# Kernel optimization log

Hardware: AMD Instinct MI355X
Metric: run time of the kernel (lower is better)

The kernel has to match this reference:

```python
import jax, jax.numpy as jnp
import numpy as np

B, L, H, W = 4, 16, 4096, 128   # W == nfeat == nclass (required by out.reshape)
NHID = 256

def setup_inputs() -> dict:
    key = jax.random.key(0)
    k1, k2, k3, k4 = jax.random.split(key, 4)
    x = jax.random.normal(k1, (B, L, H, W), dtype=jnp.float32)
    # row-normalized-ish dense adjacency stand-in for the sparse normalized adj
    adj = jax.random.uniform(k2, (H, H), dtype=jnp.float32) / H
    # GraphConvolution params: support = input @ Wk; out = adj @ support + bk
    W1 = jax.random.normal(k3, (W, NHID), dtype=jnp.float32) / np.sqrt(W)
    b1 = jnp.zeros((NHID,), dtype=jnp.float32)
    W2 = jax.random.normal(k4, (NHID, W), dtype=jnp.float32) / np.sqrt(NHID)
    b2 = jnp.zeros((W,), dtype=jnp.float32)
    return {"x": x, "adj": adj, "W1": W1, "b1": b1, "W2": W2, "b2": b2}

def reference(x, adj, W1, b1, W2, b2):
    Bv, Lv, Hv, Wv = x.shape
    xf = x.reshape(Bv * Lv, Hv, Wv)                      # [BL, H, F]
    # gc1: transform then aggregate, fused over all slices (replaces per-slice loop)
    h = jnp.einsum('nm,bmf->bnf', adj, xf @ W1) + b1     # [BL, H, nhid]
    h = jax.nn.relu(h)
    # dropout: inference mode (training=False) -> identity
    out = jnp.einsum('nm,bmf->bnf', adj, h @ W2) + b2    # [BL, H, nclass]
    out = out.reshape(Bv, Lv, Hv, Wv)
    return jax.nn.log_softmax(out, axis=-1)
```

## Files before the change

kernel.cpp:

```cpp
#include <hip/hip_runtime.h>

typedef __attribute__((ext_vector_type(4))) float f32x4;
typedef __attribute__((ext_vector_type(16))) float f32x16;
typedef __attribute__((ext_vector_type(4))) int i32x4;
typedef __attribute__((ext_vector_type(8))) int i32x8;
typedef union { i32x8 v8; i32x4 v4[2]; } opnd;

__device__ __forceinline__ unsigned fp4q(float v) {
  float a = __builtin_fabsf(v);
  unsigned q = (unsigned)(a > 0.25f) + (a > 0.75f) + (a > 1.25f) + (a > 1.75f)
             + (a > 2.5f) + (a > 3.5f) + (a > 5.0f);
  return q | (v < 0.0f ? 8u : 0u);
}

#if __has_builtin(__builtin_amdgcn_cvt_scalef32_pk_fp4_f32)
#define PKFP4(old, x, y, s) __builtin_amdgcn_cvt_scalef32_pk_fp4_f32((old), (x), (y), 1.0f, (s))
#else
#define PKFP4(old, x, y, s) ((old) | ((fp4q(x) | (fp4q(y) << 4)) << (8 * (s))))
#endif

__device__ __forceinline__ long tiled_addr(long r, long k, int nkb) {
  return (((r >> 5) * nkb) + (k >> 6)) * 2048 + ((k & 16) ? 1024 : 0)
       + (((r & 31) + (((k >> 5) & 1) << 5)) << 4) + (k & 15);
}
__device__ __forceinline__ long tile4_addr(long r, long k, int nkb) {
  return (((r >> 5) * nkb) + (k >> 6)) * 1024
       + (((r & 31) + (((k >> 5) & 1) << 5)) << 4) + ((k & 31) >> 1);
}

__device__ __forceinline__ long remap_wg(int lin, int nwg, int gx) {
  long g = lin;
  if ((nwg & 7) == 0) {
    int cpx = nwg >> 3;
    int gyx = cpx / gx;
    int xcd = lin & 7, idx = lin >> 3;
    if ((gx & 3) == 0 && gyx >= 4 && (gyx & 3) == 0) {
      int st = idx >> 4, wi = idx & 15;
      int nstr = gx >> 2;
      int str = st % nstr, stc = st / nstr;
      int r = str * 4 + (wi & 3);
      int c2 = stc * 4 + (wi >> 2);
      g = (long)xcd * cpx + (long)c2 * gx + r;
    } else {
      g = (long)xcd * cpx + idx;
    }
  }
  return g;
}

__global__ __launch_bounds__(256) void cvtAdj4t(const float* __restrict__ in,
                                                unsigned char* __restrict__ out, long n) {
  long i = ((long)blockIdx.x * 256 + threadIdx.x) * 8;
  if (i >= n) return;
  float4 a = *(const float4*)(in + i);
  float4 b = *(const float4*)(in + i + 4);
  const float S = 24576.0f;
  unsigned word = PKFP4(0u, a.x * S, a.y * S, 0);
  word = PKFP4(word, a.z * S, a.w * S, 1);
  word = PKFP4(word, b.x * S, b.y * S, 2);
  word = PKFP4(word, b.z * S, b.w * S, 3);
  long r = i >> 12;
  long k = i & 4095;
  *(int*)(out + tile4_addr(r, k, 64)) = (int)word;
}

__global__ __launch_bounds__(256) void cvtX4t(const float* __restrict__ X,
                                              unsigned char* __restrict__ out4) {
  __shared__ float tile[32][33];
  const int tid = threadIdx.x;
  const long bl = blockIdx.z;
  const int m0 = blockIdx.y * 32;
  const int w0 = blockIdx.x * 32;
  const float* xb = X + (bl * 4096 + m0) * 128 + w0;
  int row = tid >> 3, cg = tid & 7;
  float4 v = *(const float4*)(xb + (long)row * 128 + cg * 4);
  tile[row][cg * 4 + 0] = v.x;
  tile[row][cg * 4 + 1] = v.y;
  tile[row][cg * 4 + 2] = v.z;
  tile[row][cg * 4 + 3] = v.w;
  __syncthreads();
  if (tid < 128) {
    int wv = tid & 31, mg = tid >> 5;
    float t[8];
#pragma unroll
    for (int i = 0; i < 8; ++i) t[i] = tile[mg * 8 + i][wv];
    unsigned word = PKFP4(0u, t[0], t[1], 0);
    word = PKFP4(word, t[2], t[3], 1);
    word = PKFP4(word, t[4], t[5], 2);
    word = PKFP4(word, t[6], t[7], 3);
    long r = bl * 128 + w0 + wv;
    long k = m0 + mg * 8;
    *(int*)(out4 + tile4_addr(r, k, 64)) = (int)word;
  }
}

__global__ __launch_bounds__(256) void prep_params(const float* __restrict__ W1,
                                                   const float* __restrict__ W2,
                                                   unsigned char* __restrict__ W1T8,
                                                   unsigned char* __restrict__ W2T8) {
  int idx = blockIdx.x * 256 + threadIdx.x;
  if (idx < 32768) {
    int f = idx >> 7, wv = idx & 127;
    float v = W1[wv * 256 + f] * 16.0f;
    int pk = __builtin_amdgcn_cvt_pk_fp8_f32(v, v, 0, 0);
    W1T8[tiled_addr(f, wv, 2)] = (unsigned char)(pk & 0xff);
  } else {
    int t = idx - 32768;
    int cc = t >> 8, f = t & 255;
    float v = W2[f * 128 + cc] * 16.0f;
    int pk = __builtin_amdgcn_cvt_pk_fp8_f32(v, v, 0, 0);
    W2T8[tiled_addr(cc, f, 4)] = (unsigned char)(pk & 0xff);
  }
}

__global__ __launch_bounds__(256, 3) void gemmS1(const unsigned char* __restrict__ A4,
                                                 const unsigned char* __restrict__ X4,
                                                 const unsigned char* __restrict__ W1T8,
                                                 const unsigned char* __restrict__ W2T8,
                                                 unsigned char* __restrict__ t2T4,
                                                 const float* __restrict__ b1,
                                                 int K, int gx) {
  __shared__ unsigned char lds[49152];
  const int tid = threadIdx.x;
  const int l = tid & 63;
  const int w = tid >> 6;
  long g = remap_wg(blockIdx.x, gridDim.x, gx);
  const long row0 = (g % gx) * 128;
  const long bl = g / gx;
  const int nkb = K >> 6;
  const int wr = w >> 1, wc = w & 1;
  const unsigned char* sAp = A4 + (((row0 >> 5) + w) * (long)nkb) * 1024 + l * 16;
  const unsigned char* sXp = X4 + ((bl * 4 + w) * (long)nkb) * 1024 + l * 16;
  unsigned char* ldsw = lds + w * 1024;
  const unsigned char* rA = lds + (wr * 2) * 1024 + l * 16;
  const unsigned char* rX = lds + 4096 + (wc * 2) * 1024 + l * 16;

  f32x16 acc[2][2] = {};
  opnd aE[2], xE[2], aO[2], xO[2];
  const i32x4 z4 = {0, 0, 0, 0};
#pragma unroll
  for (int fi = 0; fi < 2; ++fi) {
    aE[fi].v4[1] = z4; xE[fi].v4[1] = z4;
    aO[fi].v4[1] = z4; xO[fi].v4[1] = z4;
  }

#define STG(B, SL) do { long o0_ = (long)(2 * (B)) * 1024; long o1_ = o0_ + 1024;     \
    unsigned char* d_ = ldsw + (SL) * 16384;                                          \
    __builtin_amdgcn_global_load_lds((const unsigned int*)(const void*)(sAp + o0_),   \
                                     (unsigned int*)(d_), 16, 0, 0);                  \
    __builtin_amdgcn_global_load_lds((const unsigned int*)(const void*)(sXp + o0_),   \
                                     (unsigned int*)(d_ + 4096), 16, 0, 0);           \
    __builtin_amdgcn_global_load_lds((const unsigned int*)(const void*)(sAp + o1_),   \
                                     (unsigned int*)(d_ + 8192), 16, 0, 0);           \
    __builtin_amdgcn_global_load_lds((const unsigned int*)(const void*)(sXp + o1_),   \
                                     (unsigned int*)(d_ + 12288), 16, 0, 0);          \
  } while (0)
#define LDF(SL, HALF, AV, XV) do { const long s_ = (SL) * 16384 + (HALF) * 8192;      \
    AV[0].v4[0] = *(const i32x4*)(rA + s_);                                           \
    AV[1].v4[0] = *(const i32x4*)(rA + s_ + 1024);                                    \
    XV[0].v4[0] = *(const i32x4*)(rX + s_);                                           \
    XV[1].v4[0] = *(const i32x4*)(rX + s_ + 1024); } while (0)
#define MFMAS(AV, XV) do {                                                            \
    __builtin_amdgcn_s_setprio(1);                                                    \
    _Pragma("unroll") for (int fi = 0; fi < 2; ++fi)                                  \
      _Pragma("unroll") for (int j = 0; j < 2; ++j)                                   \
        acc[fi][j] = __builtin_amdgcn_mfma_scale_f32_32x32x64_f8f6f4(                 \
            XV[j].v8, AV[fi].v8, acc[fi][j], 4, 4, 0, 127, 0, 124);                   \
    __builtin_amdgcn_s_setprio(0); } while (0)
#define BODYS(SL, SS, DOSTG, B, N) do {                                               \
    LDF(SL, 0, aE, xE);                                                               \
    if (DOSTG) STG((B) + 2, SS);                                                      \
    LDF(SL, 1, aO, xO);                                                               \
    MFMAS(aE, xE);                                                                    \
    MFMAS(aO, xO);                                                                    \
    asm volatile("s_waitcnt vmcnt(" N ")" ::: "memory");                              \
    __builtin_amdgcn_s_barrier(); } while (0)

  STG(0, 0); STG(1, 1);
  asm volatile("s_waitcnt vmcnt(4)" ::: "memory");
  __builtin_amdgcn_s_barrier();
  for (int b = 0; b < 30; b += 3) {
    BODYS(0, 2, 1, b + 0, "4");
    BODYS(1, 0, 1, b + 1, "4");
    BODYS(2, 1, 1, b + 2, "4");
  }
  BODYS(0, 0, 0, 30, "0");
  BODYS(1, 0, 0, 31, "0");
#undef STG
#undef LDF
#undef MFMAS
#undef BODYS

  unsigned char* S1buf = lds;
  unsigned char* hbuf = lds + 16384;

  const int hi = l >> 5;
  const int ln = l & 31;
#pragma unroll
  for (int fi = 0; fi < 2; ++fi) {
    int n = (wr * 2 + fi) * 32 + ln;
#pragma unroll
    for (int j = 0; j < 2; ++j) {
      int wb = (wc * 2 + j) * 32 + 4 * hi;
#pragma unroll
      for (int r4 = 0; r4 < 4; ++r4) {
        int w0 = wb + 8 * r4;
        int word = __builtin_amdgcn_cvt_pk_fp8_f32(acc[fi][j][4 * r4 + 0],
                                                   acc[fi][j][4 * r4 + 1], 0, false);
        word = __builtin_amdgcn_cvt_pk_fp8_f32(acc[fi][j][4 * r4 + 2],
                                               acc[fi][j][4 * r4 + 3], word, true);
        *(int*)(S1buf + tiled_addr(n, w0, 2)) = word;
      }
    }
  }
  __syncthreads();

  const float c1 = 128.0f / 49152.0f;
#pragma unroll
  for (int hh = 0; hh < 2; ++hh) {
#pragma unroll
    for (int fi = 0; fi < 2; ++fi)
#pragma unroll
      for (int jb = 0; jb < 2; ++jb) acc[fi][jb] = (f32x16){};
#pragma unroll
    for (int kt1 = 0; kt1 < 2; ++kt1) {
#pragma unroll
      for (int jb = 0; jb < 2; ++jb) {
        opnd aw;
        const unsigned char* pW = W1T8 + (long)((hh * 4 + wc * 2 + jb) * 2 + kt1) * 2048 + l * 16;
        aw.v4[0] = *(const i32x4*)(pW);
        aw.v4[1] = *(const i32x4*)(pW + 1024);
#pragma unroll
        for (int fi = 0; fi < 2; ++fi) {
          opnd bs;
          const unsigned char* pS = S1buf + (long)((wr * 2 + fi) * 2 + kt1) * 2048 + l * 16;
          bs.v4[0] = *(const i32x4*)(pS);
          bs.v4[1] = *(const i32x4*)(pS + 1024);
          acc[fi][jb] = __builtin_amdgcn_mfma_scale_f32_32x32x64_f8f6f4(
              aw.v8, bs.v8, acc[fi][jb], 0, 0, 0, 127, 0, 127);
        }
      }
    }
#pragma unroll
    for (int jb = 0; jb < 2; ++jb) {
      int fb = (hh * 4 + wc * 2 + jb) * 32 + 4 * hi;
#pragma unroll
      for (int r4 = 0; r4 < 4; ++r4) {
        int f0 = fb + 8 * r4;
        float4 bb = *(const float4*)(b1 + f0);
#pragma unroll
        for (int fi = 0; fi < 2; ++fi) {
          int n = (wr * 2 + fi) * 32 + ln;
          float v0 = fmaxf(fmaf(acc[fi][jb][4 * r4 + 0], c1, bb.x * 128.0f), 0.0f);
          float v1 = fmaxf(fmaf(acc[fi][jb][4 * r4 + 1], c1, bb.y * 128.0f), 0.0f);
          float v2 = fmaxf(fmaf(acc[fi][jb][4 * r4 + 2], c1, bb.z * 128.0f), 0.0f);
          float v3 = fmaxf(fmaf(acc[fi][jb][4 * r4 + 3], c1, bb.w * 128.0f), 0.0f);
          int word = __builtin_amdgcn_cvt_pk_fp8_f32(v0, v1, 0, false);
          word = __builtin_amdgcn_cvt_pk_fp8_f32(v2, v3, word, true);
          *(int*)(hbuf + tiled_addr(n, f0, 4)) = word;
        }
      }
    }
  }
  __syncthreads();

#pragma unroll
  for (int fi = 0; fi < 2; ++fi)
#pragma unroll
    for (int jb = 0; jb < 2; ++jb) acc[fi][jb] = (f32x16){};
#pragma unroll
  for (int kt2 = 0; kt2 < 4; ++kt2) {
#pragma unroll
    for (int jb = 0; jb < 2; ++jb) {
      opnd bw;
      const unsigned char* pW = W2T8 + (long)((wc * 2 + jb) * 4 + kt2) * 2048 + l * 16;
      bw.v4[0] = *(const i32x4*)(pW);
      bw.v4[1] = *(const i32x4*)(pW + 1024);
#pragma unroll
      for (int fi = 0; fi < 2; ++fi) {
        opnd ah;
        const unsigned char* pH = hbuf + (long)((wr * 2 + fi) * 4 + kt2) * 2048 + l * 16;
        ah.v4[0] = *(const i32x4*)(pH);
        ah.v4[1] = *(const i32x4*)(pH + 1024);
        acc[fi][jb] = __builtin_amdgcn_mfma_scale_f32_32x32x64_f8f6f4(
            ah.v8, bw.v8, acc[fi][jb], 0, 0, 0, 127, 0, 127);
      }
    }
  }
  unsigned char* ob = t2T4 + bl * 262144;
#pragma unroll
  for (int fi = 0; fi < 2; ++fi) {
#pragma unroll
    for (int jb = 0; jb < 2; ++jb) {
      int cc = wc * 64 + jb * 32 + ln;
#pragma unroll
      for (int run = 0; run < 4; ++run) {
        long n0 = row0 + wr * 64 + fi * 32 + 8 * run + 4 * hi;
        const float s = 0.125f;
        unsigned pkw = PKFP4(0u, acc[fi][jb][run * 4 + 0] * s,
                                 acc[fi][jb][run * 4 + 1] * s, 0);
        pkw = PKFP4(pkw, acc[fi][jb][run * 4 + 2] * s,
                         acc[fi][jb][run * 4 + 3] * s, 1);
        *(ushort*)(ob + tile4_addr(cc, n0, 64)) = (ushort)pkw;
      }
    }
  }
}

__global__ __launch_bounds__(256, 3) void gemm256sm(const unsigned char* __restrict__ A4,
                                                    const unsigned char* __restrict__ B4,
                                                    float* __restrict__ out,
                                                    const float* __restrict__ bias,
                                                    float ooScale, int K, int gx,
                                                    int chunkBase) {
  __shared__ unsigned char lds[49152];
  const int tid = threadIdx.x;
  const int l = tid & 63;
  const int w = tid >> 6;
  long g = remap_wg(blockIdx.x, gridDim.x, gx);
  const long row0 = (g % gx) * 128;
  const long bl = g / gx;
  const int nkb = K >> 6;
  const unsigned char* sAp = A4 + (((row0 >> 5) + w) * (long)nkb) * 1024 + l * 16;
  const unsigned char* sXp = B4 + ((bl * 4 + w) * (long)nkb) * 1024 + l * 16;
  unsigned char* ldsw = lds + w * 1024;
  const unsigned char* rA = lds + w * 1024 + l * 16;
  const unsigned char* rB = lds + 4096 + l * 16;

  f32x16 acc[4] = {};
  opnd aE, aO, bE[4], bO[4];
  const i32x4 z4 = {0, 0, 0, 0};
  aE.v4[1] = z4; aO.v4[1] = z4;
#pragma unroll
  for (int j = 0; j < 4; ++j) { bE[j].v4[1] = z4; bO[j].v4[1] = z4; }

#define STG(B, SL) do { long o0_ = (long)(2 * (B)) * 1024; long o1_ = o0_ + 1024;     \
    unsigned char* d_ = ldsw + (SL) * 16384;                                          \
    __builtin_amdgcn_global_load_lds((const unsigned int*)(const void*)(sAp + o0_),   \
                                     (unsigned int*)(d_), 16, 0, 0);                  \
    __builtin_amdgcn_global_load_lds((const unsigned int*)(const void*)(sXp + o0_),   \
                                     (unsigned int*)(d_ + 4096), 16, 0, 0);           \
    __builtin_amdgcn_global_load_lds((const unsigned int*)(const void*)(sAp + o1_),   \
                                     (unsigned int*)(d_ + 8192), 16, 0, 0);           \
    __builtin_amdgcn_global_load_lds((const unsigned int*)(const void*)(sXp + o1_),   \
                                     (unsigned int*)(d_ + 12288), 16, 0, 0);          \
  } while (0)
#define LDF(SL, HALF, AV, BV) do { const long s_ = (SL) * 16384 + (HALF) * 8192;      \
    AV.v4[0] = *(const i32x4*)(rA + s_);                                              \
    BV[0].v4[0] = *(const i32x4*)(rB + s_);                                           \
    BV[1].v4[0] = *(const i32x4*)(rB + s_ + 1024);                                    \
    BV[2].v4[0] = *(const i32x4*)(rB + s_ + 2048);                                    \
    BV[3].v4[0] = *(const i32x4*)(rB + s_ + 3072); } while (0)
#define MFMAS(AV, BV) do {                                                            \
    __builtin_amdgcn_s_setprio(1);                                                    \
    _Pragma("unroll") for (int j = 0; j < 4; ++j)                                     \
      acc[j] = __builtin_amdgcn_mfma_scale_f32_32x32x64_f8f6f4(                       \
          AV.v8, BV[j].v8, acc[j], 4, 4, 0, 127, 0, 127);                             \
    __builtin_amdgcn_s_setprio(0); } while (0)
#define BODYS(SL, SS, DOSTG, B, N) do {                                               \
    LDF(SL, 0, aE, bE);                                                               \
    if (DOSTG) STG((B) + 2, SS);                                                      \
    LDF(SL, 1, aO, bO);                                                               \
    MFMAS(aE, bE);                                                                    \
    MFMAS(aO, bO);                                                                    \
    asm volatile("s_waitcnt vmcnt(" N ")" ::: "memory");                              \
    __builtin_amdgcn_s_barrier(); } while (0)

  STG(0, 0); STG(1, 1);
  asm volatile("s_waitcnt vmcnt(4)" ::: "memory");
  __builtin_amdgcn_s_barrier();
  for (int b = 0; b < 30; b += 3) {
    BODYS(0, 2, 1, b + 0, "4");
    BODYS(1, 0, 1, b + 1, "4");
    BODYS(2, 1, 1, b + 2, "4");
  }
  BODYS(0, 0, 0, 30, "0");
  BODYS(1, 0, 0, 31, "0");
#undef STG
#undef LDF
#undef MFMAS
#undef BODYS

  const int hi = l >> 5;
  float bb[4];
#pragma unroll
  for (int j = 0; j < 4; ++j) bb[j] = bias[j * 32 + (l & 31)];
#pragma unroll
  for (int rr = 0; rr < 16; ++rr) {
    float v0 = acc[0][rr] * ooScale + bb[0];
    float v1 = acc[1][rr] * ooScale + bb[1];
    float v2 = acc[2][rr] * ooScale + bb[2];
    float v3 = acc[3][rr] * ooScale + bb[3];
    float m = fmaxf(fmaxf(v0, v1), fmaxf(v2, v3));
#pragma unroll
    for (int o = 16; o > 0; o >>= 1) m = fmaxf(m, __shfl_xor(m, o));
    float s = __expf(v0 - m) + __expf(v1 - m) + __expf(v2 - m) + __expf(v3 - m);
#pragma unroll
    for (int o = 16; o > 0; o >>= 1) s += __shfl_xor(s, o);
    float lse = m + __logf(s);
    long row = row0 + w * 32 + ((rr & 3) + 8 * (rr >> 2) + 4 * hi);
    float* dst = out + ((long)(chunkBase + bl) * 4096 + row) * 128;
    dst[(l & 31)] = v0 - lse;
    dst[32 + (l & 31)] = v1 - lse;
    dst[64 + (l & 31)] = v2 - lse;
    dst[96 + (l & 31)] = v3 - lse;
  }
}

extern "C" void kernel_launch(void* const* d_in, const int* in_sizes, int n_in,
                              void* d_out, int out_size, void* d_ws, size_t ws_size,
                              hipStream_t stream) {
  const float* x = (const float*)d_in[0];
  const float* adj = (const float*)d_in[1];
  const float* W1 = (const float*)d_in[2];
  const float* b1 = (const float*)d_in[3];
  const float* W2 = (const float*)d_in[4];
  const float* b2 = (const float*)d_in[5];
  float* out = (float*)d_out;
  char* ws = (char*)d_ws;

  unsigned char* adj4 = (unsigned char*)ws;
  unsigned char* W1T8 = (unsigned char*)(ws + 8388608);
  unsigned char* W2T8 = (unsigned char*)(ws + 8388608 + 32768);
  const size_t base = 9ull * 1024 * 1024;

  const int cands[6] = {64, 32, 16, 8, 4, 2};
  int c = 2;
  for (int t = 0; t < 6; ++t) {
    size_t need = base + (size_t)cands[t] * 524288;
    if (need <= ws_size) { c = cands[t]; break; }
  }
  unsigned char* x4T = (unsigned char*)(ws + base);
  unsigned char* t2T4 = x4T + (size_t)c * 262144;

  cvtAdj4t<<<8192, 256, 0, stream>>>(adj, adj4, (long)4096 * 4096);
  prep_params<<<256, 256, 0, stream>>>(W1, W2, W1T8, W2T8);

  int chunks = 64 / c;
  for (int cb = 0; cb < chunks; ++cb) {
    int base_bl = cb * c;
    const float* xc = x + (long)base_bl * 4096 * 128;

    cvtX4t<<<dim3(4, 128, c), 256, 0, stream>>>(xc, x4T);
    gemmS1<<<32 * c, 256, 0, stream>>>(adj4, x4T, W1T8, W2T8, t2T4, b1, 4096, 32);
    gemm256sm<<<32 * c, 256, 0, stream>>>(adj4, t2T4, out, b2,
                                          1.0f / 6291456.0f, 4096, 32, base_bl);
  }
}
```

Baseline: 236.2 us.

## Load A operand directly to registers and shrink LDS ring for B

Restructures the FP4 MFMA GEMM main loop: A tiles are no longer staged through LDS but loaded straight from global into registers two k-steps ahead, while B tiles use a 4-slot 16KB LDS ring with 3-deep prefetch. LDS per block drops from 48KB to 16KB and launch bounds are raised to 4 blocks per CU for higher occupancy. The waitcnt accounting now mixes direct register loads with LDS loads, which risks mis-synchronisation or exposed global latency on the A path. The loop count is hardcoded to 64 k-tiles.

Measured after the change: 232.9 us. No clear change (-1.4%).

```diff
diff --git a/kernel.cpp b/kernel.cpp
--- a/kernel.cpp
+++ b/kernel.cpp
@@ -307,13 +307,13 @@
   }
 }
 
-__global__ __launch_bounds__(256, 3) void gemm256sm(const unsigned char* __restrict__ A4,
+__global__ __launch_bounds__(256, 4) void gemm256sm(const unsigned char* __restrict__ A4,
                                                     const unsigned char* __restrict__ B4,
                                                     float* __restrict__ out,
                                                     const float* __restrict__ bias,
                                                     float ooScale, int K, int gx,
                                                     int chunkBase) {
-  __shared__ unsigned char lds[49152];
+  __shared__ unsigned char ring[16384];
   const int tid = threadIdx.x;
   const int l = tid & 63;
   const int w = tid >> 6;
@@ -321,65 +321,58 @@
   const long row0 = (g % gx) * 128;
   const long bl = g / gx;
   const int nkb = K >> 6;
-  const unsigned char* sAp = A4 + (((row0 >> 5) + w) * (long)nkb) * 1024 + l * 16;
-  const unsigned char* sXp = B4 + ((bl * 4 + w) * (long)nkb) * 1024 + l * 16;
-  unsigned char* ldsw = lds + w * 1024;
-  const unsigned char* rA = lds + w * 1024 + l * 16;
-  const unsigned char* rB = lds + 4096 + l * 16;
+  const unsigned char* sBp = B4 + ((bl * 4 + w) * (long)nkb) * 1024 + l * 16;
+  unsigned char* ringw = ring + w * 1024;
+  const unsigned char* rB = ring + l * 16;
+  const unsigned char* pA = A4 + (((row0 >> 5) + w) * (long)nkb) * 1024 + l * 16;
 
   f32x16 acc[4] = {};
-  opnd aE, aO, bE[4], bO[4];
+  opnd av0, av1, bv[4];
   const i32x4 z4 = {0, 0, 0, 0};
-  aE.v4[1] = z4; aO.v4[1] = z4;
-#pragma unroll
-  for (int j = 0; j < 4; ++j) { bE[j].v4[1] = z4; bO[j].v4[1] = z4; }
-
-#define STG(B, SL) do { long o0_ = (long)(2 * (B)) * 1024; long o1_ = o0_ + 1024;     \
-    unsigned char* d_ = ldsw + (SL) * 16384;                                          \
-    __builtin_amdgcn_global_load_lds((const unsigned int*)(const void*)(sAp + o0_),   \
-                                     (unsigned int*)(d_), 16, 0, 0);                  \
-    __builtin_amdgcn_global_load_lds((const unsigned int*)(const void*)(sXp + o0_),   \
-                                     (unsigned int*)(d_ + 4096), 16, 0, 0);           \
-    __builtin_amdgcn_global_load_lds((const unsigned int*)(const void*)(sAp + o1_),   \
-                                     (unsigned int*)(d_ + 8192), 16, 0, 0);           \
-    __builtin_amdgcn_global_load_lds((const unsigned int*)(const void*)(sXp + o1_),   \
-                                     (unsigned int*)(d_ + 12288), 16, 0, 0);          \
-  } while (0)
-#define LDF(SL, HALF, AV, BV) do { const long s_ = (SL) * 16384 + (HALF) * 8192;      \
-    AV.v4[0] = *(const i32x4*)(rA + s_);                                              \
-    BV[0].v4[0] = *(const i32x4*)(rB + s_);                                           \
-    BV[1].v4[0] = *(const i32x4*)(rB + s_ + 1024);                                    \
-    BV[2].v4[0] = *(const i32x4*)(rB + s_ + 2048);                                    \
-    BV[3].v4[0] = *(const i32x4*)(rB + s_ + 3072); } while (0)
-#define MFMAS(AV, BV) do {                                                            \
-    __builtin_amdgcn_s_setprio(1);                                                    \
+  av0.v4[1] = z4; av1.v4[1] = z4;
+#pragma unroll
+  for (int j = 0; j < 4; ++j) bv[j].v4[1] = z4;
+
+#define STGB(KT) __builtin_amdgcn_global_load_lds(                                    \
+    (const unsigned int*)(const void*)(sBp + (long)(KT) * 1024),                      \
+    (unsigned int*)(ringw + (((KT) & 3) << 12)), 16, 0, 0)
+#define LOADA(KT, AV) AV.v4[0] = *(const i32x4*)(pA + (long)(KT) * 1024)
+#define LDB(KT) do { const unsigned char* p_ = rB + (((KT) & 3) << 12);               \
+    bv[0].v4[0] = *(const i32x4*)(p_);                                                \
+    bv[1].v4[0] = *(const i32x4*)(p_ + 1024);                                         \
+    bv[2].v4[0] = *(const i32x4*)(p_ + 2048);                                         \
+    bv[3].v4[0] = *(const i32x4*)(p_ + 3072); } while (0)
+#define MFMAS(AV) do { __builtin_amdgcn_s_setprio(1);                                 \
     _Pragma("unroll") for (int j = 0; j < 4; ++j)                                     \
       acc[j] = __builtin_amdgcn_mfma_scale_f32_32x32x64_f8f6f4(                       \
-          AV.v8, BV[j].v8, acc[j], 4, 4, 0, 127, 0, 127);                             \
+          AV.v8, bv[j].v8, acc[j], 4, 4, 0, 127, 0, 127);                             \
     __builtin_amdgcn_s_setprio(0); } while (0)
-#define BODYS(SL, SS, DOSTG, B, N) do {                                               \
-    LDF(SL, 0, aE, bE);                                                               \
-    if (DOSTG) STG((B) + 2, SS);                                                      \
-    LDF(SL, 1, aO, bO);                                                               \
-    MFMAS(aE, bE);                                                                    \
-    MFMAS(aO, bO);                                                                    \
+#define BODY(KT, N, DOSTG, DOA, AV) do {                                              \
+    LDB(KT);                                                                          \
+    if (DOSTG) STGB((KT) + 3);                                                        \
     asm volatile("s_waitcnt vmcnt(" N ")" ::: "memory");                              \
+    MFMAS(AV);                                                                        \
+    if (DOA) LOADA((KT) + 2, AV);                                                     \
     __builtin_amdgcn_s_barrier(); } while (0)
 
-  STG(0, 0); STG(1, 1);
-  asm volatile("s_waitcnt vmcnt(4)" ::: "memory");
-  __builtin_amdgcn_s_barrier();
-  for (int b = 0; b < 30; b += 3) {
-    BODYS(0, 2, 1, b + 0, "4");
-    BODYS(1, 0, 1, b + 1, "4");
-    BODYS(2, 1, 1, b + 2, "4");
-  }
-  BODYS(0, 0, 0, 30, "0");
-  BODYS(1, 0, 0, 31, "0");
-#undef STG
-#undef LDF
+  const int nkt = K >> 6;
+  STGB(0); LOADA(0, av0); STGB(1); LOADA(1, av1); STGB(2);
+
+  BODY(0, "4", 1, 1, av0);
+  BODY(1, "4", 1, 1, av1);
+  for (int kt = 2; kt <= 58; kt += 2) {
+    BODY(kt,     "3", 1, 1, av0);
+    BODY(kt + 1, "3", 1, 1, av1);
+  }
+  BODY(60, "3", 1, 1, av0);
+  BODY(61, "2", 0, 1, av1);
+  BODY(62, "1", 0, 0, av0);
+  BODY(63, "0", 0, 0, av1);
+#undef STGB
+#undef LOADA
+#undef LDB
 #undef MFMAS
-#undef BODYS
+#undef BODY
 
   const int hi = l >> 5;
   float bb[4];
```
